# Kernel optimization log

Measured on AMD Instinct MI355X. Metric: run time of the kernel, lower is better.

The kernel has to match this reference:

```python
import jax, jax.numpy as jnp
import numpy as np

B, S, D, H, E, TOP_K = 4, 2048, 1024, 2048, 8, 2


def setup_inputs() -> dict:
    key = jax.random.key(0)
    ks = jax.random.split(key, 5)
    scale_d = 1.0 / np.sqrt(D)
    scale_h = 1.0 / np.sqrt(H)
    return {
        "x": jax.random.normal(ks[0], (B, S, D), dtype=jnp.float32),
        "gate_w": jax.random.normal(ks[1], (D, E), dtype=jnp.float32) * scale_d,
        "w1": jax.random.normal(ks[2], (E, D, H), dtype=jnp.float32) * scale_d,
        "w2": jax.random.normal(ks[3], (E, D, H), dtype=jnp.float32) * scale_d,
        "w3": jax.random.normal(ks[4], (E, H, D), dtype=jnp.float32) * scale_h,
    }


def reference(x, gate_w, w1, w2, w3):
    # Gating: softmax over experts, keep top-k probs, renormalize.
    gate_scores = jax.nn.softmax(x @ gate_w, axis=-1)          # [B,S,E]
    top_vals, top_idx = jax.lax.top_k(gate_scores, TOP_K)      # [B,S,K]
    mask = (jax.nn.one_hot(top_idx, E, dtype=x.dtype) * top_vals[..., None]).sum(axis=-2)  # [B,S,E]
    weights = mask / (mask.sum(axis=-1, keepdims=True) + 1e-9)
    # Dense SwiGLU over ALL experts (faithful to the original ModuleList loop).
    g = jax.nn.silu(jnp.einsum('bsd,edh->bseh', x, w1)) * jnp.einsum('bsd,edh->bseh', x, w2)  # [B,S,E,H]
    expert_out = jnp.einsum('bseh,ehd->bsed', g, w3)           # [B,S,E,D]
    # Masked weighted combine (dropout is identity in eval / p=0).
    return jnp.einsum('bse,bsed->bsd', weights, expert_out)    # [B,S,D]
```

## Files before the change

### kernel.cpp

```cpp
#include <hip/hip_runtime.h>

#define T_TOK 8192
#define DDIM 1024
#define HDIM 2048
#define NEXP 8

typedef __attribute__((ext_vector_type(8))) short short8;
typedef __attribute__((ext_vector_type(4))) float f32x4;

#define WAITV8 asm volatile("s_waitcnt vmcnt(8)" ::: "memory")
#define WAITV6 asm volatile("s_waitcnt vmcnt(6)" ::: "memory")
#define WAITV0 asm volatile("s_waitcnt vmcnt(0)" ::: "memory")
#define WAITL0 asm volatile("s_waitcnt lgkmcnt(0)" ::: "memory")
#define BARRIER __builtin_amdgcn_s_barrier()

__device__ __forceinline__ unsigned short f2bf(float f) {
  unsigned int u = __builtin_bit_cast(unsigned int, f);
  u += 0x7fffu + ((u >> 16) & 1u);
  return (unsigned short)(u >> 16);
}
__device__ __forceinline__ float bf2f(unsigned short h) {
  unsigned int u = ((unsigned int)h) << 16;
  return __builtin_bit_cast(float, u);
}
__device__ __forceinline__ void gload16(const void* g, void* l) {
  __builtin_amdgcn_global_load_lds((const __attribute__((address_space(1))) void*)g,
                                   (__attribute__((address_space(3))) void*)l, 16, 0, 0);
}
__device__ __forceinline__ int imin(int a, int b) { return a < b ? a : b; }

__global__ __launch_bounds__(256) void tcvt_kernel(const float* __restrict__ in,
                                                   unsigned short* __restrict__ out,
                                                   int R, int C, size_t outEstride,
                                                   int perm, int s16) {
  int e = blockIdx.z;
  int rb = blockIdx.y * 64, cb = blockIdx.x * 64;
  const float* inE = in + (size_t)e * R * C;
  unsigned short* outE = out + (size_t)e * outEstride;
  __shared__ float tile[64][65];
  int tid = threadIdx.x;
  #pragma unroll
  for (int i = 0; i < 4; ++i) {
    int f = tid + i * 256;
    int r = f >> 4, c4 = (f & 15) << 2;
    float4 v = *(const float4*)(inE + (size_t)(rb + r) * C + cb + c4);
    tile[r][c4] = v.x; tile[r][c4 + 1] = v.y; tile[r][c4 + 2] = v.z; tile[r][c4 + 3] = v.w;
  }
  __syncthreads();
  #pragma unroll
  for (int i = 0; i < 2; ++i) {
    int g = tid + i * 256;
    int oc = g >> 3;
    int r8 = (g & 7) << 3;
    alignas(16) unsigned short tmp[8];
    #pragma unroll
    for (int j = 0; j < 8; ++j) tmp[j] = f2bf(tile[r8 + j][oc]);
    int orow = cb + oc;
    int orow2 = perm ? (32 * (orow >> 4) + (orow & 15) + s16) : orow;
    *(uint4*)(outE + (size_t)orow2 * R + rb + r8) = *(const uint4*)tmp;
  }
}

__global__ __launch_bounds__(256) void gate_kernel(const float* __restrict__ x,
                                                   const float* __restrict__ gw,
                                                   int* __restrict__ t_exp,
                                                   float* __restrict__ t_w,
                                                   unsigned short* __restrict__ xbf) {
  int t = blockIdx.x * 4 + (threadIdx.x >> 6);
  int lane = threadIdx.x & 63;
  const float* xp = x + (size_t)t * DDIM;
  unsigned short* xo = xbf + (size_t)t * DDIM;
  float acc[NEXP];
  #pragma unroll
  for (int e = 0; e < NEXP; ++e) acc[e] = 0.f;
  for (int i = 0; i < DDIM / 64; ++i) {
    int d = i * 64 + lane;
    float xv = xp[d];
    xo[d] = f2bf(xv);
    const float* g = gw + d * NEXP;
    #pragma unroll
    for (int e = 0; e < NEXP; ++e) acc[e] += xv * g[e];
  }
  #pragma unroll
  for (int off = 32; off > 0; off >>= 1) {
    #pragma unroll
    for (int e = 0; e < NEXP; ++e) acc[e] += __shfl_xor(acc[e], off, 64);
  }
  float mx = acc[0];
  #pragma unroll
  for (int e = 1; e < NEXP; ++e) mx = fmaxf(mx, acc[e]);
  float p[NEXP]; float S = 0.f;
  #pragma unroll
  for (int e = 0; e < NEXP; ++e) { p[e] = expf(acc[e] - mx); S += p[e]; }
  int i0 = 0; float v0 = p[0];
  #pragma unroll
  for (int e = 1; e < NEXP; ++e) if (p[e] > v0) { v0 = p[e]; i0 = e; }
  int i1 = -1; float v1 = -1.f;
  #pragma unroll
  for (int e = 0; e < NEXP; ++e) if (e != i0 && p[e] > v1) { v1 = p[e]; i1 = e; }
  float pv0 = v0 / S, pv1 = v1 / S;
  float denom = pv0 + pv1 + 1e-9f;
  if (lane == 0) {
    t_exp[t * 2] = i0; t_exp[t * 2 + 1] = i1;
    t_w[t * 2] = pv0 / denom; t_w[t * 2 + 1] = pv1 / denom;
  }
}

__global__ __launch_bounds__(1024) void partition_kernel(
    const int* __restrict__ t_exp, const float* __restrict__ t_w,
    int* __restrict__ ctrl, int* __restrict__ row_tok,
    float* __restrict__ row_w, int* __restrict__ inv_row,
    int* __restrict__ tmap) {
  int tid = threadIdx.x;
  int wv = tid >> 6, lane = tid & 63;
  __shared__ int wtot[16][8];
  __shared__ int wbase[16][8];
  __shared__ int soff[8];

  int t0 = tid * 8;
  int exps[16];
  int c[8];
  #pragma unroll
  for (int e = 0; e < 8; ++e) c[e] = 0;
  #pragma unroll
  for (int s = 0; s < 16; ++s) {
    exps[s] = t_exp[t0 * 2 + s];
    #pragma unroll
    for (int e = 0; e < 8; ++e) c[e] += (exps[s] == e);
  }
  int inc[8];
  #pragma unroll
  for (int e = 0; e < 8; ++e) inc[e] = c[e];
  #pragma unroll
  for (int d = 1; d < 64; d <<= 1) {
    #pragma unroll
    for (int e = 0; e < 8; ++e) {
      int v = __shfl_up(inc[e], d, 64);
      if (lane >= d) inc[e] += v;
    }
  }
  if (lane == 63) {
    #pragma unroll
    for (int e = 0; e < 8; ++e) wtot[wv][e] = inc[e];
  }
  __syncthreads();
  if (wv == 0 && lane < 16) {
    #pragma unroll
    for (int e = 0; e < 8; ++e) {
      int b = 0;
      for (int w = 0; w < 16; ++w)
        if (w < lane) b += wtot[w][e];
      wbase[lane][e] = b;
    }
  }
  __syncthreads();
  if (tid == 0) {
    int o = 0;
    #pragma unroll
    for (int e = 0; e < 8; ++e) {
      int tot = wbase[15][e] + wtot[15][e];
      ctrl[e] = tot; ctrl[8 + e] = o; soff[e] = o; o += tot;
    }
  }
  __syncthreads();
  int base[8];
  #pragma unroll
  for (int e = 0; e < 8; ++e) base[e] = soff[e] + wbase[wv][e] + (inc[e] - c[e]);
  #pragma unroll
  for (int s = 0; s < 16; ++s) {
    int ee = exps[s];
    float w = t_w[t0 * 2 + s];
    int pos = 0;
    #pragma unroll
    for (int e = 0; e < 8; ++e)
      if (ee == e) { pos = base[e]; base[e] = base[e] + 1; }
    row_tok[pos] = t0 + (s >> 1);
    row_w[pos] = w;
    inv_row[t0 * 2 + s] = pos;
  }
  __syncthreads();
  if (tid == 0) {
    int T1 = 0, T2 = 0;
    for (int e = 0; e < 8; ++e) {
      int cnt = ctrl[e];
      int n1 = (cnt + 255) >> 8;
      for (int m = 0; m < n1; ++m) tmap[T1++] = (e << 8) | m;
    }
    for (int e = 0; e < 8; ++e) {
      int cnt = ctrl[e];
      int n2 = (cnt + 127) >> 7;
      for (int m = 0; m < n2; ++m) tmap[128 + T2++] = (e << 8) | m;
    }
    ctrl[16] = T1; ctrl[17] = T2;
  }
}


#define KSTEP(T_, NT_) do {                                                \
    int buf_ = (T_) & 3;                                                   \
    WAITV8;                                                                \
    BARRIER;                                                               \
    int tc_ = imin((T_) + 3, (NT_) - 1);                                   \
    STG(tc_ & 3, tc_);                                                     \
    short8 av[8], bv[4];                                                   \
    _Pragma("unroll")                                                      \
    for (int n = 0; n < 4; ++n)                                            \
      bv[n] = *(const short8*)(&lds[buf_][1][0] + bOff + n * 512);         \
    _Pragma("unroll")                                                      \
    for (int m = 0; m < 8; ++m)                                            \
      av[m] = *(const short8*)(&lds[buf_][0][0] + aOff + m * 512);         \
    __builtin_amdgcn_s_setprio(1);                                         \
    _Pragma("unroll")                                                      \
    for (int m = 0; m < 8; ++m)                                            \
      _Pragma("unroll")                                                    \
      for (int n = 0; n < 4; ++n)                                          \
        acc[m][n] = __builtin_amdgcn_mfma_f32_16x16x32_bf16(av[m], bv[n], acc[m][n], 0, 0, 0); \
    __builtin_amdgcn_s_setprio(0);                                         \
    WAITL0;                                                                \
} while (0)

#define K_PIPELINE(NT_)                                                    \
  WAITV0;                                                                  \
  STG(0, 0); STG(1, 1); STG(2, 2);                                         \
  _Pragma("unroll 1")                                                      \
  for (int t = 0; t < (NT_); ++t) { KSTEP(t, (NT_)); }

__global__ __launch_bounds__(512, 1) void gemm1_kernel(
    const unsigned short* __restrict__ xbf,
    const unsigned short* __restrict__ w12t,
    const int* __restrict__ row_tok, const float* __restrict__ row_w,
    const int* __restrict__ ctrl, const int* __restrict__ tmap,
    unsigned short* __restrict__ G) {
  int bid = blockIdx.x;
  int nt = bid & 15;
  int ti = bid >> 4;
  if (ti >= ctrl[16]) return;
  int pm = tmap[ti];
  int e = pm >> 8, mt = pm & 255;
  int cnt = ctrl[e];
  int off = ctrl[8 + e];

  __shared__ unsigned short lds[4][2][8192];

  int tid = threadIdx.x, lane = tid & 63;
  const unsigned short* w12e = w12t + (size_t)e * (4096 * 1024);

  int sr = tid >> 2;
  int cS8 = ((tid & 3) ^ ((sr >> 1) & 3)) * 8;
  const unsigned short* bQ0 = w12e + (size_t)(nt * 256 + sr) * 1024 + cS8;
  const unsigned short* bQ1 = w12e + (size_t)(nt * 256 + 128 + sr) * 1024 + cS8;

  int wid = tid >> 6, wr = wid >> 2, wc = wid & 3;
  int lr16 = lane & 15, hi = lane >> 4;
  int koff = (hi ^ ((lr16 >> 1) & 3)) * 8;
  int aOff = (wr * 128 + lr16) * 32 + koff;
  int bOff = (wc * 64 + lr16) * 32 + koff;

  int tokA = row_tok[off + imin(mt * 256 + sr, cnt - 1)];
  int tokB = row_tok[off + imin(mt * 256 + 128 + sr, cnt - 1)];
  const unsigned short* aQ0 = xbf + (size_t)tokA * 1024 + cS8;
  const unsigned short* aQ1 = xbf + (size_t)tokB * 1024 + cS8;

#define STG(SB, T_) do {                                                   \
    gload16(aQ0 + (T_) * 32, &lds[SB][0][0] + tid * 8);                    \
    gload16(aQ1 + (T_) * 32, &lds[SB][0][0] + 4096 + tid * 8);             \
    gload16(bQ0 + (T_) * 32, &lds[SB][1][0] + tid * 8);                    \
    gload16(bQ1 + (T_) * 32, &lds[SB][1][0] + 4096 + tid * 8); } while (0)

  f32x4 z = {0.f, 0.f, 0.f, 0.f};
  f32x4 acc[8][4];
  #pragma unroll
  for (int m = 0; m < 8; ++m)
    #pragma unroll
    for (int n = 0; n < 4; ++n) acc[m][n] = z;

  K_PIPELINE(32)

  #pragma unroll
  for (int m = 0; m < 8; ++m)
    #pragma unroll
    for (int jj = 0; jj < 4; ++jj) {
      int rl = mt * 256 + wr * 128 + m * 16 + hi * 4 + jj;
      if (rl < cnt) {
        float wrj = row_w[off + rl];
        size_t base = (size_t)(off + rl) * HDIM + nt * 128 + wc * 32 + lr16;
        float h1 = acc[m][0][jj], h2 = acc[m][1][jj];
        G[base] = f2bf((h1 / (1.f + __expf(-h1))) * h2 * wrj);
        h1 = acc[m][2][jj]; h2 = acc[m][3][jj];
        G[base + 16] = f2bf((h1 / (1.f + __expf(-h1))) * h2 * wrj);
      }
    }
#undef STG
}

__global__ __launch_bounds__(512, 1) void gemm2_kernel(
    const unsigned short* __restrict__ G,
    const unsigned short* __restrict__ w3t,
    const int* __restrict__ ctrl, const int* __restrict__ tmap,
    unsigned short* __restrict__ Y) {
  int bid = blockIdx.x;
  int nt = bid & 3;
  int ti = bid >> 2;
  if (ti >= ctrl[17]) return;
  int pm = tmap[ti];
  int e = pm >> 8, mt = pm & 255;
  int cnt = ctrl[e];
  int off = ctrl[8 + e];

  __shared__ unsigned short ldsA[4][4096];
  __shared__ unsigned short ldsB[4][8192];

  int tid = threadIdx.x, lane = tid & 63;
  const unsigned short* w3e = w3t + (size_t)e * (1024 * 2048);

  int sr = tid >> 2;
  int cS8 = ((tid & 3) ^ ((sr >> 1) & 3)) * 8;
  const unsigned short* bQ0 = w3e + (size_t)(nt * 256 + sr) * 2048 + cS8;
  const unsigned short* bQ1 = w3e + (size_t)(nt * 256 + 128 + sr) * 2048 + cS8;
  const unsigned short* aQ0 =
      G + (size_t)(off + imin(mt * 128 + sr, cnt - 1)) * 2048 + cS8;

  int wid = tid >> 6, wr = wid >> 2, wc = wid & 3;
  int lr16 = lane & 15, hi = lane >> 4;
  int koff = (hi ^ ((lr16 >> 1) & 3)) * 8;
  int aOff = (wr * 64 + lr16) * 32 + koff;
  int bOff = (wc * 64 + lr16) * 32 + koff;

#define STG2(SB, T_) do {                                                  \
    gload16(aQ0 + (T_) * 32, &ldsA[SB][0] + tid * 8);                      \
    gload16(bQ0 + (T_) * 32, &ldsB[SB][0] + tid * 8);                      \
    gload16(bQ1 + (T_) * 32, &ldsB[SB][0] + 4096 + tid * 8); } while (0)

  f32x4 z = {0.f, 0.f, 0.f, 0.f};
  f32x4 acc[4][4];
  #pragma unroll
  for (int m = 0; m < 4; ++m)
    #pragma unroll
    for (int n = 0; n < 4; ++n) acc[m][n] = z;

  WAITV0;
  STG2(0, 0); STG2(1, 1); STG2(2, 2);
  #pragma unroll 1
  for (int t = 0; t < 64; ++t) {
    int buf = t & 3;
    WAITV6;
    BARRIER;
    int tc = imin(t + 3, 63);
    STG2(tc & 3, tc);
    short8 av[4], bv[4];
    #pragma unroll
    for (int n = 0; n < 4; ++n)
      bv[n] = *(const short8*)(&ldsB[buf][0] + bOff + n * 512);
    #pragma unroll
    for (int m = 0; m < 4; ++m)
      av[m] = *(const short8*)(&ldsA[buf][0] + aOff + m * 512);
    __builtin_amdgcn_s_setprio(1);
    #pragma unroll
    for (int m = 0; m < 4; ++m)
      #pragma unroll
      for (int n = 0; n < 4; ++n)
        acc[m][n] = __builtin_amdgcn_mfma_f32_16x16x32_bf16(av[m], bv[n], acc[m][n], 0, 0, 0);
    __builtin_amdgcn_s_setprio(0);
    WAITL0;
  }
#undef STG2

  #pragma unroll
  for (int m = 0; m < 4; ++m)
    #pragma unroll
    for (int jj = 0; jj < 4; ++jj) {
      int rl = mt * 128 + wr * 64 + m * 16 + hi * 4 + jj;
      if (rl < cnt) {
        size_t yrow = (size_t)(off + rl) * DDIM + nt * 256 + wc * 64 + lr16;
        #pragma unroll
        for (int n = 0; n < 4; ++n) Y[yrow + n * 16] = f2bf(acc[m][n][jj]);
      }
    }
}

__global__ __launch_bounds__(256) void combine_kernel(const unsigned short* __restrict__ Y,
                                                      const int* __restrict__ inv_row,
                                                      float* __restrict__ out) {
  int gid = blockIdx.x * 256 + threadIdx.x;
  int t = gid >> 7;
  int cidx = (gid & 127) * 8;
  int rA = inv_row[t * 2], rB = inv_row[t * 2 + 1];
  uint4 va = *(const uint4*)(Y + (size_t)rA * DDIM + cidx);
  uint4 vb = *(const uint4*)(Y + (size_t)rB * DDIM + cidx);
  const unsigned short* pa = (const unsigned short*)&va;
  const unsigned short* pb = (const unsigned short*)&vb;
  float4 o0, o1;
  o0.x = bf2f(pa[0]) + bf2f(pb[0]); o0.y = bf2f(pa[1]) + bf2f(pb[1]);
  o0.z = bf2f(pa[2]) + bf2f(pb[2]); o0.w = bf2f(pa[3]) + bf2f(pb[3]);
  o1.x = bf2f(pa[4]) + bf2f(pb[4]); o1.y = bf2f(pa[5]) + bf2f(pb[5]);
  o1.z = bf2f(pa[6]) + bf2f(pb[6]); o1.w = bf2f(pa[7]) + bf2f(pb[7]);
  float* op = out + (size_t)t * DDIM + cidx;
  *(float4*)op = o0;
  *(float4*)(op + 4) = o1;
}

extern "C" void kernel_launch(void* const* d_in, const int* in_sizes, int n_in,
                              void* d_out, int out_size, void* d_ws, size_t ws_size,
                              hipStream_t stream) {
  const float* x  = (const float*)d_in[0];
  const float* gw = (const float*)d_in[1];
  const float* w1 = (const float*)d_in[2];
  const float* w2 = (const float*)d_in[3];
  const float* w3 = (const float*)d_in[4];
  float* out = (float*)d_out;
  char* ws = (char*)d_ws;

  unsigned short* xbf  = (unsigned short*)(ws + 0);
  unsigned short* w12t = (unsigned short*)(ws + 16777216);
  unsigned short* w3t  = (unsigned short*)(ws + 83886080);
  unsigned short* G    = (unsigned short*)(ws + 117440512);
  unsigned short* Y    = (unsigned short*)(ws + 184549376);
  int*   row_tok = (int*)  (ws + 218103808);
  float* row_w   = (float*)(ws + 218169344);
  int*   inv_row = (int*)  (ws + 218234880);
  int*   t_exp   = (int*)  (ws + 218300416);
  float* t_w     = (float*)(ws + 218365952);
  int*   ctrl    = (int*)  (ws + 218431488);

  tcvt_kernel<<<dim3(32, 16, 8), 256, 0, stream>>>(w1, w12t, 1024, 2048,
                                                   (size_t)4096 * 1024, 1, 0);
  tcvt_kernel<<<dim3(32, 16, 8), 256, 0, stream>>>(w2, w12t, 1024, 2048,
                                                   (size_t)4096 * 1024, 1, 16);
  tcvt_kernel<<<dim3(16, 32, 8), 256, 0, stream>>>(w3, w3t, 2048, 1024,
                                                   (size_t)1024 * 2048, 0, 0);

  gate_kernel<<<2048, 256, 0, stream>>>(x, gw, t_exp, t_w, xbf);
  partition_kernel<<<1, 1024, 0, stream>>>(t_exp, t_w, ctrl, row_tok, row_w,
                                           inv_row, t_exp);

  gemm1_kernel<<<1152, 512, 0, stream>>>(xbf, w12t, row_tok, row_w, ctrl, t_exp, G);
  gemm2_kernel<<<544, 512, 0, stream>>>(G, w3t, ctrl, t_exp + 128, Y);
  combine_kernel<<<4096, 256, 0, stream>>>(Y, inv_row, out);
}
```

Before: 446.5 us.

## Use persistent atomic work-queue GEMMs, fuse weight conversions, parallelize tile map

```diff
diff --git a/kernel.cpp b/kernel.cpp
--- a/kernel.cpp
+++ b/kernel.cpp
@@ -29,14 +29,27 @@
 }
 __device__ __forceinline__ int imin(int a, int b) { return a < b ? a : b; }
 
-__global__ __launch_bounds__(256) void tcvt_kernel(const float* __restrict__ in,
-                                                   unsigned short* __restrict__ out,
-                                                   int R, int C, size_t outEstride,
-                                                   int perm, int s16) {
-  int e = blockIdx.z;
-  int rb = blockIdx.y * 64, cb = blockIdx.x * 64;
-  const float* inE = in + (size_t)e * R * C;
-  unsigned short* outE = out + (size_t)e * outEstride;
+__global__ __launch_bounds__(256) void tcvt_all_kernel(const float* __restrict__ w1,
+                                                       const float* __restrict__ w2,
+                                                       const float* __restrict__ w3,
+                                                       unsigned short* __restrict__ w12t,
+                                                       unsigned short* __restrict__ w3t) {
+  int z = blockIdx.z;
+  const float* inE; unsigned short* outE;
+  int R, C, perm, s16, rb, cb;
+  if (z < 16) {
+    int e = z & 7;
+    inE = (z < 8 ? w1 : w2) + (size_t)e * 1024 * 2048;
+    outE = w12t + (size_t)e * 4096 * 1024;
+    R = 1024; C = 2048; perm = 1; s16 = (z < 8) ? 0 : 16;
+    rb = blockIdx.y * 64; cb = blockIdx.x * 64;
+  } else {
+    int e = z - 16;
+    inE = w3 + (size_t)e * 2048 * 1024;
+    outE = w3t + (size_t)e * 1024 * 2048;
+    R = 2048; C = 1024; perm = 0; s16 = 0;
+    rb = blockIdx.x * 64; cb = blockIdx.y * 64;
+  }
   __shared__ float tile[64][65];
   int tid = threadIdx.x;
   #pragma unroll
@@ -179,19 +192,20 @@
     inv_row[t0 * 2 + s] = pos;
   }
   __syncthreads();
-  if (tid == 0) {
-    int T1 = 0, T2 = 0;
-    for (int e = 0; e < 8; ++e) {
-      int cnt = ctrl[e];
-      int n1 = (cnt + 255) >> 8;
-      for (int m = 0; m < n1; ++m) tmap[T1++] = (e << 8) | m;
+  if (wv == 0 && lane < 8) {
+    int cnt = ctrl[lane];
+    int n1 = (cnt + 255) >> 8, n2 = (cnt + 127) >> 7;
+    int p1 = n1, p2 = n2;
+    #pragma unroll
+    for (int d = 1; d < 8; d <<= 1) {
+      int v1 = __shfl_up(p1, d, 64);
+      int v2 = __shfl_up(p2, d, 64);
+      if (lane >= d) { p1 += v1; p2 += v2; }
     }
-    for (int e = 0; e < 8; ++e) {
-      int cnt = ctrl[e];
-      int n2 = (cnt + 127) >> 7;
-      for (int m = 0; m < n2; ++m) tmap[128 + T2++] = (e << 8) | m;
-    }
-    ctrl[16] = T1; ctrl[17] = T2;
+    int b1 = p1 - n1, b2 = p2 - n2;
+    for (int m = 0; m < n1; ++m) tmap[b1 + m] = (lane << 8) | m;
+    for (int m = 0; m < n2; ++m) tmap[128 + b2 + m] = (lane << 8) | m;
+    if (lane == 7) { ctrl[16] = p1; ctrl[17] = p2; ctrl[18] = 0; ctrl[19] = 0; }
   }
 }
 
@@ -229,37 +243,40 @@
     const unsigned short* __restrict__ xbf,
     const unsigned short* __restrict__ w12t,
     const int* __restrict__ row_tok, const float* __restrict__ row_w,
-    const int* __restrict__ ctrl, const int* __restrict__ tmap,
+    int* __restrict__ ctrl, const int* __restrict__ tmap,
     unsigned short* __restrict__ G) {
-  int bid = blockIdx.x;
-  int nt = bid & 15;
-  int ti = bid >> 4;
-  if (ti >= ctrl[16]) return;
-  int pm = tmap[ti];
-  int e = pm >> 8, mt = pm & 255;
-  int cnt = ctrl[e];
-  int off = ctrl[8 + e];
-
   __shared__ unsigned short lds[4][2][8192];
+  __shared__ int s_item;
 
   int tid = threadIdx.x, lane = tid & 63;
-  const unsigned short* w12e = w12t + (size_t)e * (4096 * 1024);
-
   int sr = tid >> 2;
   int cS8 = ((tid & 3) ^ ((sr >> 1) & 3)) * 8;
-  const unsigned short* bQ0 = w12e + (size_t)(nt * 256 + sr) * 1024 + cS8;
-  const unsigned short* bQ1 = w12e + (size_t)(nt * 256 + 128 + sr) * 1024 + cS8;
-
   int wid = tid >> 6, wr = wid >> 2, wc = wid & 3;
   int lr16 = lane & 15, hi = lane >> 4;
   int koff = (hi ^ ((lr16 >> 1) & 3)) * 8;
   int aOff = (wr * 128 + lr16) * 32 + koff;
   int bOff = (wc * 64 + lr16) * 32 + koff;
-
-  int tokA = row_tok[off + imin(mt * 256 + sr, cnt - 1)];
-  int tokB = row_tok[off + imin(mt * 256 + 128 + sr, cnt - 1)];
-  const unsigned short* aQ0 = xbf + (size_t)tokA * 1024 + cS8;
-  const unsigned short* aQ1 = xbf + (size_t)tokB * 1024 + cS8;
+  int total = ctrl[16] << 4;
+
+  for (;;) {
+    BARRIER;
+    if (tid == 0) s_item = atomicAdd(&ctrl[18], 1);
+    BARRIER;
+    int item = s_item;
+    if (item >= total) break;
+    int nt = item & 15, ti = item >> 4;
+    int pm = tmap[ti];
+    int e = pm >> 8, mt = pm & 255;
+    int cnt = ctrl[e];
+    int off = ctrl[8 + e];
+
+    const unsigned short* w12e = w12t + (size_t)e * (4096 * 1024);
+    const unsigned short* bQ0 = w12e + (size_t)(nt * 256 + sr) * 1024 + cS8;
+    const unsigned short* bQ1 = w12e + (size_t)(nt * 256 + 128 + sr) * 1024 + cS8;
+    int tokA = row_tok[off + imin(mt * 256 + sr, cnt - 1)];
+    int tokB = row_tok[off + imin(mt * 256 + 128 + sr, cnt - 1)];
+    const unsigned short* aQ0 = xbf + (size_t)tokA * 1024 + cS8;
+    const unsigned short* aQ1 = xbf + (size_t)tokB * 1024 + cS8;
 
 #define STG(SB, T_) do {                                                   \
     gload16(aQ0 + (T_) * 32, &lds[SB][0][0] + tid * 8);                    \
@@ -267,115 +284,121 @@
     gload16(bQ0 + (T_) * 32, &lds[SB][1][0] + tid * 8);                    \
     gload16(bQ1 + (T_) * 32, &lds[SB][1][0] + 4096 + tid * 8); } while (0)
 
-  f32x4 z = {0.f, 0.f, 0.f, 0.f};
-  f32x4 acc[8][4];
-  #pragma unroll
-  for (int m = 0; m < 8; ++m)
-    #pragma unroll
-    for (int n = 0; n < 4; ++n) acc[m][n] = z;
-
-  K_PIPELINE(32)
-
-  #pragma unroll
-  for (int m = 0; m < 8; ++m)
-    #pragma unroll
-    for (int jj = 0; jj < 4; ++jj) {
-      int rl = mt * 256 + wr * 128 + m * 16 + hi * 4 + jj;
-      if (rl < cnt) {
-        float wrj = row_w[off + rl];
-        size_t base = (size_t)(off + rl) * HDIM + nt * 128 + wc * 32 + lr16;
-        float h1 = acc[m][0][jj], h2 = acc[m][1][jj];
-        G[base] = f2bf((h1 / (1.f + __expf(-h1))) * h2 * wrj);
-        h1 = acc[m][2][jj]; h2 = acc[m][3][jj];
-        G[base + 16] = f2bf((h1 / (1.f + __expf(-h1))) * h2 * wrj);
+    f32x4 z = {0.f, 0.f, 0.f, 0.f};
+    f32x4 acc[8][4];
+    #pragma unroll
+    for (int m = 0; m < 8; ++m)
+      #pragma unroll
+      for (int n = 0; n < 4; ++n) acc[m][n] = z;
+
+    K_PIPELINE(32)
+
+    #pragma unroll
+    for (int m = 0; m < 8; ++m)
+      #pragma unroll
+      for (int jj = 0; jj < 4; ++jj) {
+        int rl = mt * 256 + wr * 128 + m * 16 + hi * 4 + jj;
+        if (rl < cnt) {
+          float wrj = row_w[off + rl];
+          size_t base = (size_t)(off + rl) * HDIM + nt * 128 + wc * 32 + lr16;
+          float h1 = acc[m][0][jj], h2 = acc[m][1][jj];
+          G[base] = f2bf((h1 / (1.f + __expf(-h1))) * h2 * wrj);
+          h1 = acc[m][2][jj]; h2 = acc[m][3][jj];
+          G[base + 16] = f2bf((h1 / (1.f + __expf(-h1))) * h2 * wrj);
+        }
       }
-    }
 #undef STG
+  }
 }
 
 __global__ __launch_bounds__(512, 1) void gemm2_kernel(
     const unsigned short* __restrict__ G,
     const unsigned short* __restrict__ w3t,
-    const int* __restrict__ ctrl, const int* __restrict__ tmap,
+    int* __restrict__ ctrl, const int* __restrict__ tmap,
     unsigned short* __restrict__ Y) {
-  int bid = blockIdx.x;
-  int nt = bid & 3;
-  int ti = bid >> 2;
-  if (ti >= ctrl[17]) return;
-  int pm = tmap[ti];
-  int e = pm >> 8, mt = pm & 255;
-  int cnt = ctrl[e];
-  int off = ctrl[8 + e];
-
   __shared__ unsigned short ldsA[4][4096];
   __shared__ unsigned short ldsB[4][8192];
+  __shared__ int s_item;
 
   int tid = threadIdx.x, lane = tid & 63;
-  const unsigned short* w3e = w3t + (size_t)e * (1024 * 2048);
-
   int sr = tid >> 2;
   int cS8 = ((tid & 3) ^ ((sr >> 1) & 3)) * 8;
-  const unsigned short* bQ0 = w3e + (size_t)(nt * 256 + sr) * 2048 + cS8;
-  const unsigned short* bQ1 = w3e + (size_t)(nt * 256 + 128 + sr) * 2048 + cS8;
-  const unsigned short* aQ0 =
-      G + (size_t)(off + imin(mt * 128 + sr, cnt - 1)) * 2048 + cS8;
-
   int wid = tid >> 6, wr = wid >> 2, wc = wid & 3;
   int lr16 = lane & 15, hi = lane >> 4;
   int koff = (hi ^ ((lr16 >> 1) & 3)) * 8;
   int aOff = (wr * 64 + lr16) * 32 + koff;
   int bOff = (wc * 64 + lr16) * 32 + koff;
+  int total = ctrl[17] << 2;
+
+  for (;;) {
+    BARRIER;
+    if (tid == 0) s_item = atomicAdd(&ctrl[19], 1);
+    BARRIER;
+    int item = s_item;
+    if (item >= total) break;
+    int nt = item & 3, ti = item >> 2;
+    int pm = tmap[ti];
+    int e = pm >> 8, mt = pm & 255;
+    int cnt = ctrl[e];
+    int off = ctrl[8 + e];
+
+    const unsigned short* w3e = w3t + (size_t)e * (1024 * 2048);
+    const unsigned short* bQ0 = w3e + (size_t)(nt * 256 + sr) * 2048 + cS8;
+    const unsigned short* bQ1 = w3e + (size_t)(nt * 256 + 128 + sr) * 2048 + cS8;
+    const unsigned short* aQ0 =
+        G + (size_t)(off + imin(mt * 128 + sr, cnt - 1)) * 2048 + cS8;
 
 #define STG2(SB, T_) do {                                                  \
     gload16(aQ0 + (T_) * 32, &ldsA[SB][0] + tid * 8);                      \
     gload16(bQ0 + (T_) * 32, &ldsB[SB][0] + tid * 8);                      \
     gload16(bQ1 + (T_) * 32, &ldsB[SB][0] + 4096 + tid * 8); } while (0)
 
-  f32x4 z = {0.f, 0.f, 0.f, 0.f};
-  f32x4 acc[4][4];
-  #pragma unroll
-  for (int m = 0; m < 4; ++m)
-    #pragma unroll
-    for (int n = 0; n < 4; ++n) acc[m][n] = z;
-
-  WAITV0;
-  STG2(0, 0); STG2(1, 1); STG2(2, 2);
-  #pragma unroll 1
-  for (int t = 0; t < 64; ++t) {
-    int buf = t & 3;
-    WAITV6;
-    BARRIER;
-    int tc = imin(t + 3, 63);
-    STG2(tc & 3, tc);
-    short8 av[4], bv[4];
-    #pragma unroll
-    for (int n = 0; n < 4; ++n)
-      bv[n] = *(const short8*)(&ldsB[buf][0] + bOff + n * 512);
+    f32x4 z = {0.f, 0.f, 0.f, 0.f};
+    f32x4 acc[4][4];
     #pragma unroll
     for (int m = 0; m < 4; ++m)
-      av[m] = *(const short8*)(&ldsA[buf][0] + aOff + m * 512);
-    __builtin_amdgcn_s_setprio(1);
+      #pragma unroll
+      for (int n = 0; n < 4; ++n) acc[m][n] = z;
+
+    WAITV0;
+    STG2(0, 0); STG2(1, 1); STG2(2, 2);
+    #pragma unroll 1
+    for (int t = 0; t < 64; ++t) {
+      int buf = t & 3;
+      WAITV6;
+      BARRIER;
+      int tc = imin(t + 3, 63);
+      STG2(tc & 3, tc);
+      short8 av[4], bv[4];
+      #pragma unroll
+      for (int n = 0; n < 4; ++n)
+        bv[n] = *(const short8*)(&ldsB[buf][0] + bOff + n * 512);
+      #pragma unroll
+      for (int m = 0; m < 4; ++m)
+        av[m] = *(const short8*)(&ldsA[buf][0] + aOff + m * 512);
+      __builtin_amdgcn_s_setprio(1);
+      #pragma unroll
+      for (int m = 0; m < 4; ++m)
+        #pragma unroll
+        for (int n = 0; n < 4; ++n)
+          acc[m][n] = __builtin_amdgcn_mfma_f32_16x16x32_bf16(av[m], bv[n], acc[m][n], 0, 0, 0);
+      __builtin_amdgcn_s_setprio(0);
+      WAITL0;
+    }
+#undef STG2
+
     #pragma unroll
     for (int m = 0; m < 4; ++m)
       #pragma unroll
-      for (int n = 0; n < 4; ++n)
-        acc[m][n] = __builtin_amdgcn_mfma_f32_16x16x32_bf16(av[m], bv[n], acc[m][n], 0, 0, 0);
-    __builtin_amdgcn_s_setprio(0);
-    WAITL0;
-  }
-#undef STG2
-
-  #pragma unroll
-  for (int m = 0; m < 4; ++m)
-    #pragma unroll
-    for (int jj = 0; jj < 4; ++jj) {
-      int rl = mt * 128 + wr * 64 + m * 16 + hi * 4 + jj;
-      if (rl < cnt) {
-        size_t yrow = (size_t)(off + rl) * DDIM + nt * 256 + wc * 64 + lr16;
-        #pragma unroll
-        for (int n = 0; n < 4; ++n) Y[yrow + n * 16] = f2bf(acc[m][n][jj]);
+      for (int jj = 0; jj < 4; ++jj) {
+        int rl = mt * 128 + wr * 64 + m * 16 + hi * 4 + jj;
+        if (rl < cnt) {
+          size_t yrow = (size_t)(off + rl) * DDIM + nt * 256 + wc * 64 + lr16;
+          #pragma unroll
+          for (int n = 0; n < 4; ++n) Y[yrow + n * 16] = f2bf(acc[m][n][jj]);
+        }
       }
-    }
+  }
 }
 
 __global__ __launch_bounds__(256) void combine_kernel(const unsigned short* __restrict__ Y,
@@ -422,18 +445,13 @@
   float* t_w     = (float*)(ws + 218365952);
   int*   ctrl    = (int*)  (ws + 218431488);
 
-  tcvt_kernel<<<dim3(32, 16, 8), 256, 0, stream>>>(w1, w12t, 1024, 2048,
-                                                   (size_t)4096 * 1024, 1, 0);
-  tcvt_kernel<<<dim3(32, 16, 8), 256, 0, stream>>>(w2, w12t, 1024, 2048,
-                                                   (size_t)4096 * 1024, 1, 16);
-  tcvt_kernel<<<dim3(16, 32, 8), 256, 0, stream>>>(w3, w3t, 2048, 1024,
-                                                   (size_t)1024 * 2048, 0, 0);
+  tcvt_all_kernel<<<dim3(32, 16, 24), 256, 0, stream>>>(w1, w2, w3, w12t, w3t);
 
   gate_kernel<<<2048, 256, 0, stream>>>(x, gw, t_exp, t_w, xbf);
   partition_kernel<<<1, 1024, 0, stream>>>(t_exp, t_w, ctrl, row_tok, row_w,
                                            inv_row, t_exp);
 
-  gemm1_kernel<<<1152, 512, 0, stream>>>(xbf, w12t, row_tok, row_w, ctrl, t_exp, G);
-  gemm2_kernel<<<544, 512, 0, stream>>>(G, w3t, ctrl, t_exp + 128, Y);
+  gemm1_kernel<<<256, 512, 0, stream>>>(xbf, w12t, row_tok, row_w, ctrl, t_exp, G);
+  gemm2_kernel<<<256, 512, 0, stream>>>(G, w3t, ctrl, t_exp + 128, Y);
   combine_kernel<<<4096, 256, 0, stream>>>(Y, inv_row, out);
 }
```

New measurement: 493.5 us. 10.5% more time.
